# Kernel optimization log

Measured on AMD Instinct MI355X. Metric: run time of the kernel, lower is better.

The kernel has to match this reference:

```python
import jax, jax.numpy as jnp
import numpy as np
from jax import lax

N_CLASSES = 10
N_EXPERTS = 45  # 10 choose 2
EPS = 1e-5

# lookup table: (i1, i2) with i1 < i2 -> flat expert id (matches nested loop order)
_tbl = np.zeros((N_CLASSES, N_CLASSES), dtype=np.int32)
_k = 0
for _i1 in range(N_CLASSES):
    for _i2 in range(_i1 + 1, N_CLASSES):
        _tbl[_i1, _i2] = _k
        _k += 1
PAIR_TABLE = jnp.asarray(_tbl)


def _downscale(x):
    # AvgPool2d(3, stride=3) on 28x28 -> 9x9 (floor: uses top-left 27x27)
    B = x.shape[0]
    return x[:, :, :27, :27].reshape(B, 1, 9, 3, 9, 3).mean(axis=(3, 5))


def _bn_eval(h, gamma, beta, mean, var):
    scale = gamma * lax.rsqrt(var + EPS)
    return h * scale[None, :, None, None] + (beta - mean * scale)[None, :, None, None]


def _stage1(x, w1, b1, g1, be1, m1, v1, fcw1, fcb1):
    xd = _downscale(x)                                         # [B,1,9,9]
    h = lax.conv_general_dilated(xd, w1, (1, 1), 'VALID',
                                 dimension_numbers=('NCHW', 'OIHW', 'NCHW'))
    h = h + b1[None, :, None, None]                            # [B,20,7,7]
    h = _bn_eval(h, g1, be1, m1, v1)
    h = jax.nn.relu(h)
    B = h.shape[0]
    h = h[:, :, :6, :6].reshape(B, 20, 3, 2, 3, 2).max(axis=(3, 5))  # maxpool2 -> [B,20,3,3]
    h = h.reshape(B, 180)
    return h @ fcw1.T + fcb1                                   # [B,10] raw logits


def reference(x, w1, b1, g1, be1, m1, v1, fcw1, fcb1,
              w2, b2, g2, be2, m2, v2, fcw2, fcb2):
    B = x.shape[0]
    logits1 = _stage1(x, w1, b1, g1, be1, m1, v1, fcw1, fcb1)  # [B,10]
    ls1 = jax.nn.log_softmax(logits1, axis=1)

    # routing: top-2 class indices, sorted ascending, -> pairwise expert id
    top2 = jnp.sort(jnp.argsort(ls1, axis=1)[:, -2:], axis=1)  # [B,2]
    idx0, idx1 = top2[:, 0], top2[:, 1]
    eid = PAIR_TABLE[idx0, idx1]                               # [B]

    # stage 2 (TinyNet2) with per-example gathered expert params
    xd = _downscale(x)                                         # [B,1,9,9]
    # extract 5x5 conv patches (valid, stride 1): output spatial 5x5
    patches = jnp.stack([xd[:, 0, i:i + 5, j:j + 5]
                         for i in range(5) for j in range(5)], axis=1)  # [B,25,5,5]
    Wsel = w2.reshape(N_EXPERTS, 15, 25)[eid]                  # [B,15,25]
    h = jnp.einsum('bkhw,bok->bohw', patches, Wsel) + b2[eid][:, :, None, None]  # [B,15,5,5]
    scale = (g2 * lax.rsqrt(v2 + EPS))[eid]                    # [B,15]
    shift = (be2 - m2 * g2 * lax.rsqrt(v2 + EPS))[eid]
    h = h * scale[:, :, None, None] + shift[:, :, None, None]
    h = jax.nn.relu(h)
    h = h[:, :, :4, :4].reshape(B, 15, 2, 2, 2, 2).max(axis=(3, 5))  # [B,15,2,2]
    feat = h.reshape(B, 60)
    s2 = jnp.einsum('bf,bof->bo', feat, fcw2[eid]) + fcb2[eid]  # [B,2]

    # combine: scatter the two expert logits into the routed columns
    rows = jnp.arange(B)
    out = jnp.full((B, N_CLASSES), -100.0, dtype=logits1.dtype)
    out = out.at[rows, idx0].set(s2[:, 0]).at[rows, idx1].set(s2[:, 1])
    # eval-mode bypass: use stage1 raw logits if max log-prob > 0.3
    use1 = jnp.max(ls1, axis=1) > 0.3
    out = jnp.where(use1[:, None], logits1, out)
    out = jax.nn.log_softmax(out, axis=1)
    return (logits1, out)


def setup_inputs() -> dict:
    key = jax.random.key(0)
    ks = jax.random.split(key, 18)
    B = 65536
    s = 0.1
    return {
        'x': jax.random.normal(ks[0], (B, 1, 28, 28), dtype=jnp.float32),
        # stage1 (TinyNet, 20 kernels, k=3)
        'w1': jax.random.normal(ks[1], (20, 1, 3, 3), dtype=jnp.float32) * s,
        'b1': jax.random.normal(ks[2], (20,), dtype=jnp.float32) * s,
        'g1': jax.random.normal(ks[3], (20,), dtype=jnp.float32) * s + 1.0,
        'be1': jax.random.normal(ks[4], (20,), dtype=jnp.float32) * s,
        'm1': jax.random.normal(ks[5], (20,), dtype=jnp.float32) * s,
        'v1': jax.random.uniform(ks[6], (20,), dtype=jnp.float32) + 0.5,
        'fcw1': jax.random.normal(ks[7], (10, 180), dtype=jnp.float32) * s,
        'fcb1': jax.random.normal(ks[8], (10,), dtype=jnp.float32) * s,
        # 45 stacked stage2 experts (TinyNet2, 15 kernels, k=5)
        'w2': jax.random.normal(ks[9], (45, 15, 1, 5, 5), dtype=jnp.float32) * s,
        'b2': jax.random.normal(ks[10], (45, 15), dtype=jnp.float32) * s,
        'g2': jax.random.normal(ks[11], (45, 15), dtype=jnp.float32) * s + 1.0,
        'be2': jax.random.normal(ks[12], (45, 15), dtype=jnp.float32) * s,
        'm2': jax.random.normal(ks[13], (45, 15), dtype=jnp.float32) * s,
        'v2': jax.random.uniform(ks[14], (45, 15), dtype=jnp.float32) + 0.5,
        'fcw2': jax.random.normal(ks[15], (45, 2, 60), dtype=jnp.float32) * s,
        'fcb2': jax.random.normal(ks[16], (45, 2), dtype=jnp.float32) * s,
    }
```

## Files before the change

kernel.cpp:

```cpp
#include <hip/hip_runtime.h>
#include <cmath>

#define EPSF 1e-5f

#define OFF_FC2   19576
#define OFF_IMG   25088

#define I_W1P    0
#define I_FCW1R  240
#define I_B1F    2400
#define I_FCB1   2420
#define I_B2F    2432
#define I_FCB2   3108

__global__ __launch_bounds__(256) void setup_tables(
    const float* __restrict__ w1, const float* __restrict__ b1,
    const float* __restrict__ g1, const float* __restrict__ be1,
    const float* __restrict__ m1, const float* __restrict__ v1,
    const float* __restrict__ w2, const float* __restrict__ b2,
    const float* __restrict__ g2, const float* __restrict__ be2,
    const float* __restrict__ m2, const float* __restrict__ v2,
    const float* __restrict__ fcw2, const float* __restrict__ fcb2,
    const float* __restrict__ fcw1, const float* __restrict__ fcb1,
    float* __restrict__ ws)
{
  const int t  = blockIdx.x * blockDim.x + threadIdx.x;
  const int nt = gridDim.x * blockDim.x;
  float* W2F = ws;
  float* FC2 = ws + OFF_FC2;
  float* IMG = ws + OFF_IMG;

  for (int idx = t; idx < 18900; idx += nt) {
    int kk = idx & 3, rest = idx >> 2;
    int e = rest % 45, ok4 = rest / 45;
    int k4 = ok4 % 7, o = ok4 / 7;
    int k = k4 * 4 + kk;
    float s = g2[e*15+o] / sqrtf(v2[e*15+o] + EPSF);
    W2F[idx] = (k < 25) ? w2[(e*15+o)*25 + k] * s : 0.0f;
  }
  for (int idx = t; idx < 5400; idx += nt) {
    int kk = idx & 3, rest = idx >> 2;
    int e = rest % 45, t2 = rest / 45;
    int f4 = t2 % 15, oo = t2 / 15;
    FC2[idx] = fcw2[(e*2+oo)*60 + f4*4 + kk];
  }
  for (int i = t; i < 4096; i += nt) {
    float v = 0.0f;
    if (i < I_FCW1R) {
      int ch = i / 12, j = i % 12;
      if (j < 9) {
        float s = g1[ch] / sqrtf(v1[ch] + EPSF);
        v = w1[ch*9 + j] * s;
      }
    } else if (i < I_B1F) {
      int k = i - I_FCW1R;
      int c = k % 12, r2 = k / 12, pp = r2 % 9, ch = r2 / 9;
      if (c < 10) v = fcw1[c*180 + ch*9 + pp];
    } else if (i < I_FCB1) {
      int ch = i - I_B1F;
      float s = g1[ch] / sqrtf(v1[ch] + EPSF);
      v = b1[ch]*s + be1[ch] - m1[ch]*s;
    } else if (i < I_B2F) {
      int k = i - I_FCB1;
      if (k < 10) v = fcb1[k];
    } else if (i < I_FCB2) {
      int k = i - I_B2F;
      if (k < 675) {
        int e = k % 45, o = k / 45;
        float s = g2[e*15+o] / sqrtf(v2[e*15+o] + EPSF);
        v = b2[e*15+o]*s + be2[e*15+o] - m2[e*15+o]*s;
      }
    } else {
      int k = i - I_FCB2;
      if (k < 90) {
        int e = k % 45, oo = k / 45;
        v = fcb2[e*2+oo];
      }
    }
    IMG[i] = v;
  }
}

#define GETC(arr, k) ((k)%4==0 ? arr[(k)/4].x : (k)%4==1 ? arr[(k)/4].y : \
                      (k)%4==2 ? arr[(k)/4].z : arr[(k)/4].w)

#define T_RAW   4352
#define T_TAB   4352
#define SSTR    676

__global__ __attribute__((amdgpu_waves_per_eu(4, 4))) __launch_bounds__(256)
void fused_k(
    const float* __restrict__ x,
    const float* __restrict__ ws,
    float* __restrict__ out, int B)
{
  __shared__ float lds[9760];

  const int t  = threadIdx.x;
  const int p  = t & 3;
  const int sl = t >> 2;
  const int b  = blockIdx.x * 64 + sl;
  const bool valid = (b < B);

  const float4* img4 = reinterpret_cast<const float4*>(ws + OFF_IMG);
  float4 tv0 = img4[t], tv1 = img4[t + 256], tv2 = img4[t + 512], tv3 = img4[t + 768];

  const int s8  = t >> 5;
  const int tin = t & 31;

  float4 pre[6];
  {
    const int bs = blockIdx.x * 64 + s8;
    if (bs < B) {
      const float4* xp = reinterpret_cast<const float4*>(x + (size_t)bs * 784);
      #pragma unroll
      for (int j = 0; j < 5; j++) pre[j] = xp[tin + 32*j];
      pre[5] = (tin < 8) ? xp[tin + 160] : make_float4(0.f,0.f,0.f,0.f);
    } else {
      #pragma unroll
      for (int j = 0; j < 6; j++) pre[j] = make_float4(0.f,0.f,0.f,0.f);
    }
    float4* rw = reinterpret_cast<float4*>(&lds[T_RAW + s8*SSTR]);
    #pragma unroll
    for (int j = 0; j < 5; j++) rw[tin + 32*j] = pre[j];
    if (tin < 8) rw[tin + 160] = pre[5];
  }
  __syncthreads();

  #pragma unroll 1
  for (int c = 0; c < 8; c++) {
    if (c < 7) {
      const int bs = blockIdx.x * 64 + (c+1)*8 + s8;
      if (bs < B) {
        const float4* xp = reinterpret_cast<const float4*>(x + (size_t)bs * 784);
        #pragma unroll
        for (int j = 0; j < 5; j++) pre[j] = xp[tin + 32*j];
        pre[5] = (tin < 8) ? xp[tin + 160] : make_float4(0.f,0.f,0.f,0.f);
      }
    }
    if (t < 128) {
      const int ds8  = t >> 4;
      const int orow = (t >> 1) & 7;
      const int h    = t & 1;
      float a0 = 0.f, a1 = 0.f, a2 = 0.f, a3 = 0.f;
      #pragma unroll
      for (int dr = 0; dr < 3; dr++) {
        const float4* rp = reinterpret_cast<const float4*>(
            &lds[T_RAW + ds8*SSTR + (3*orow + dr)*28 + 12*h]);
        float4 q0 = rp[0], q1 = rp[1], q2 = rp[2];
        a0 += q0.x + q0.y + q0.z;
        a1 += q0.w + q1.x + q1.y;
        a2 += q1.z + q1.w + q2.x;
        a3 += q2.y + q2.z + q2.w;
      }
      float4* dst = reinterpret_cast<float4*>(&lds[(c*8 + ds8)*68 + orow*8 + 4*h]);
      *dst = make_float4(a0*(1.f/9.f), a1*(1.f/9.f), a2*(1.f/9.f), a3*(1.f/9.f));
    }
    __syncthreads();
    if (c < 7) {
      float4* rw = reinterpret_cast<float4*>(&lds[T_RAW + s8*SSTR]);
      #pragma unroll
      for (int j = 0; j < 5; j++) rw[tin + 32*j] = pre[j];
      if (tin < 8) rw[tin + 160] = pre[5];
      __syncthreads();
    }
  }

  {
    float4* tab4 = reinterpret_cast<float4*>(&lds[T_TAB]);
    tab4[t] = tv0; tab4[t + 256] = tv1; tab4[t + 512] = tv2; tab4[t + 768] = tv3;
  }

  float xd[64];
  #pragma unroll
  for (int r = 0; r < 8; r++) {
    const float4* src = reinterpret_cast<const float4*>(&lds[sl*68 + r*8]);
    float4 a = src[0], bq = src[1];
    xd[r*8+0]=a.x;  xd[r*8+1]=a.y;  xd[r*8+2]=a.z;  xd[r*8+3]=a.w;
    xd[r*8+4]=bq.x; xd[r*8+5]=bq.y; xd[r*8+6]=bq.z; xd[r*8+7]=bq.w;
  }
  __syncthreads();

  float logits[10];
  #pragma unroll
  for (int c = 0; c < 10; c++) logits[c] = 0.0f;

  #pragma unroll 1
  for (int ci = 0; ci < 5; ci++) {
    const int ch = p*5 + ci;
    const float4* wp = reinterpret_cast<const float4*>(&lds[T_TAB + I_W1P + ch*12]);
    float4 w0 = wp[0], w1v = wp[1], w2v = wp[2];
    const float w_[9] = {w0.x,w0.y,w0.z,w0.w,w1v.x,w1v.y,w1v.z,w1v.w,w2v.x};
    const float bb = lds[T_TAB + I_B1F + ch];
    float feat[9];
    #pragma unroll
    for (int pr = 0; pr < 3; pr++) {
      #pragma unroll
      for (int pc = 0; pc < 3; pc++) {
        float c00 = bb, c01 = bb, c10 = bb, c11 = bb;
        #pragma unroll
        for (int dr = 0; dr < 3; dr++) {
          #pragma unroll
          for (int dc = 0; dc < 3; dc++) {
            float wk = w_[dr*3 + dc];
            c00 = fmaf(xd[(2*pr+0+dr)*8 + 2*pc+0+dc], wk, c00);
            c01 = fmaf(xd[(2*pr+0+dr)*8 + 2*pc+1+dc], wk, c01);
            c10 = fmaf(xd[(2*pr+1+dr)*8 + 2*pc+0+dc], wk, c10);
            c11 = fmaf(xd[(2*pr+1+dr)*8 + 2*pc+1+dc], wk, c11);
          }
        }
        feat[pr*3+pc] = fmaxf(fmaxf(fmaxf(c00, c01), fmaxf(c10, c11)), 0.0f);
      }
    }
    #pragma unroll
    for (int pp = 0; pp < 9; pp++) {
      const float4* f4 = reinterpret_cast<const float4*>(&lds[T_TAB + I_FCW1R + (ch*9 + pp)*12]);
      float4 f0 = f4[0], f1 = f4[1], f2 = f4[2];
      const float fv = feat[pp];
      logits[0] = fmaf(fv, f0.x, logits[0]);
      logits[1] = fmaf(fv, f0.y, logits[1]);
      logits[2] = fmaf(fv, f0.z, logits[2]);
      logits[3] = fmaf(fv, f0.w, logits[3]);
      logits[4] = fmaf(fv, f1.x, logits[4]);
      logits[5] = fmaf(fv, f1.y, logits[5]);
      logits[6] = fmaf(fv, f1.z, logits[6]);
      logits[7] = fmaf(fv, f1.w, logits[7]);
      logits[8] = fmaf(fv, f2.x, logits[8]);
      logits[9] = fmaf(fv, f2.y, logits[9]);
    }
  }

  #pragma unroll
  for (int c = 0; c < 10; c++) {
    float v = logits[c];
    v += __shfl_xor(v, 1);
    v += __shfl_xor(v, 2);
    logits[c] = v + lds[T_TAB + I_FCB1 + c];
  }

  int i1 = 0; float v1m = logits[0];
  #pragma unroll
  for (int c = 1; c < 10; c++) { if (logits[c] >= v1m) { v1m = logits[c]; i1 = c; } }
  int i2 = 0; float v2m = -3.0e38f;
  #pragma unroll
  for (int c = 0; c < 10; c++) { if (c != i1 && logits[c] >= v2m) { v2m = logits[c]; i2 = c; } }
  const int idx0 = i1 < i2 ? i1 : i2;
  const int idx1 = i1 < i2 ? i2 : i1;
  int eid = 8*idx0 - (idx0*(idx0-1))/2 + idx1 - 1;
  eid = eid < 0 ? 0 : (eid > 44 ? 44 : eid);

  float sume = 0.0f;
  #pragma unroll
  for (int c = 0; c < 10; c++) sume += __expf(logits[c] - v1m);
  const bool use1 = (-__logf(sume)) > 0.3f;

  __syncthreads();
  if (p == 0) {
    #pragma unroll
    for (int c = 0; c < 5; c++) lds[sl*10 + c] = logits[c];
  } else if (p == 1) {
    #pragma unroll
    for (int c = 5; c < 10; c++) lds[sl*10 + c] = logits[c];
  }

  const float4* W2F4 = reinterpret_cast<const float4*>(ws);
  const float4* FC24 = reinterpret_cast<const float4*>(ws + OFF_FC2);
  float s2a = 0.0f, s2b = 0.0f;

  #pragma unroll 1
  for (int oi = 0; oi < 4; oi++) {
    const int o = p + 4*oi;
    if (o < 15) {
      float4 wv[7];
      #pragma unroll
      for (int k4 = 0; k4 < 7; k4++) wv[k4] = W2F4[(o*7 + k4)*45 + eid];
      const float bias = lds[T_TAB + I_B2F + o*45 + eid];
      const float4 fa = FC24[o*45 + eid];
      const float4 fb = FC24[(15 + o)*45 + eid];
      float feat0 = 0.f, feat1 = 0.f, feat2 = 0.f, feat3 = 0.f;
      #pragma unroll
      for (int ph = 0; ph < 2; ph++) {
        #pragma unroll
        for (int pw = 0; pw < 2; pw++) {
          float c00 = bias, c01 = bias, c10 = bias, c11 = bias;
          #pragma unroll
          for (int i = 0; i < 5; i++) {
            #pragma unroll
            for (int j = 0; j < 5; j++) {
              float wk = GETC(wv, i*5 + j);
              c00 = fmaf(xd[(2*ph+0+i)*8 + 2*pw+0+j], wk, c00);
              c01 = fmaf(xd[(2*ph+0+i)*8 + 2*pw+1+j], wk, c01);
              c10 = fmaf(xd[(2*ph+1+i)*8 + 2*pw+0+j], wk, c10);
              c11 = fmaf(xd[(2*ph+1+i)*8 + 2*pw+1+j], wk, c11);
            }
          }
          float f = fmaxf(fmaxf(fmaxf(c00, c01), fmaxf(c10, c11)), 0.0f);
          if (ph == 0 && pw == 0) feat0 = f;
          else if (ph == 0)       feat1 = f;
          else if (pw == 0)       feat2 = f;
          else                    feat3 = f;
        }
      }
      s2a = fmaf(feat0, fa.x, fmaf(feat1, fa.y, fmaf(feat2, fa.z, fmaf(feat3, fa.w, s2a))));
      s2b = fmaf(feat0, fb.x, fmaf(feat1, fb.y, fmaf(feat2, fb.z, fmaf(feat3, fb.w, s2b))));
    }
  }
  s2a += __shfl_xor(s2a, 1); s2a += __shfl_xor(s2a, 2);
  s2b += __shfl_xor(s2b, 1); s2b += __shfl_xor(s2b, 2);
  s2a += lds[T_TAB + I_FCB2 + eid];
  s2b += lds[T_TAB + I_FCB2 + 45 + eid];

  __syncthreads();
  float o10[10];
  #pragma unroll
  for (int c = 0; c < 10; c++) {
    float v = -100.0f;
    v = (c == idx0) ? s2a : v;
    v = (c == idx1) ? s2b : v;
    o10[c] = use1 ? lds[sl*10 + c] : v;
  }
  float m2x = o10[0];
  #pragma unroll
  for (int c = 1; c < 10; c++) m2x = fmaxf(m2x, o10[c]);
  float se2 = 0.0f;
  #pragma unroll
  for (int c = 0; c < 10; c++) se2 += __expf(o10[c] - m2x);
  const float lse2 = m2x + __logf(se2);

  if (p == 2) {
    #pragma unroll
    for (int c = 0; c < 5; c++) lds[640 + sl*10 + c] = o10[c] - lse2;
  } else if (p == 3) {
    #pragma unroll
    for (int c = 5; c < 10; c++) lds[640 + sl*10 + c] = o10[c] - lse2;
  }
  __syncthreads();

  if (blockIdx.x * 64 + 64 <= B) {
    const float4* l4 = reinterpret_cast<const float4*>(lds);
    const size_t o1 = (size_t)blockIdx.x * 640;
    if (t < 160)
      *reinterpret_cast<float4*>(out + o1 + (size_t)t*4) = l4[t];
    if (t >= 96)
      *reinterpret_cast<float4*>(out + (size_t)B*10 + o1 + (size_t)(t-96)*4) = l4[160 + (t-96)];
  } else if (valid) {
    const size_t base = (size_t)b * 10;
    if (p == 0) {
      #pragma unroll
      for (int c = 0; c < 5; c++) out[base + c] = lds[sl*10 + c];
    } else if (p == 1) {
      #pragma unroll
      for (int c = 5; c < 10; c++) out[base + c] = lds[sl*10 + c];
    } else if (p == 2) {
      #pragma unroll
      for (int c = 0; c < 5; c++) out[(size_t)B*10 + base + c] = lds[640 + sl*10 + c];
    } else {
      #pragma unroll
      for (int c = 5; c < 10; c++) out[(size_t)B*10 + base + c] = lds[640 + sl*10 + c];
    }
  }
}

extern "C" void kernel_launch(void* const* d_in, const int* in_sizes, int n_in,
                              void* d_out, int out_size, void* d_ws, size_t ws_size,
                              hipStream_t stream) {
  const float* x    = (const float*)d_in[0];
  const float* w1   = (const float*)d_in[1];
  const float* b1   = (const float*)d_in[2];
  const float* g1   = (const float*)d_in[3];
  const float* be1  = (const float*)d_in[4];
  const float* m1   = (const float*)d_in[5];
  const float* v1   = (const float*)d_in[6];
  const float* fcw1 = (const float*)d_in[7];
  const float* fcb1 = (const float*)d_in[8];
  const float* w2   = (const float*)d_in[9];
  const float* b2   = (const float*)d_in[10];
  const float* g2   = (const float*)d_in[11];
  const float* be2  = (const float*)d_in[12];
  const float* m2   = (const float*)d_in[13];
  const float* v2   = (const float*)d_in[14];
  const float* fcw2 = (const float*)d_in[15];
  const float* fcb2 = (const float*)d_in[16];
  float* out = (float*)d_out;
  float* ws  = (float*)d_ws;
  const int B = in_sizes[0] / 784;

  setup_tables<<<80, 256, 0, stream>>>(w1, b1, g1, be1, m1, v1,
                                       w2, b2, g2, be2, m2, v2,
                                       fcw2, fcb2, fcw1, fcb1, ws);
  fused_k<<<(B + 63)/64, 256, 0, stream>>>(x, ws, out, B);
}
```

Measured before the change: 390.1 us.

## Split work across four lanes by spatial quadrant instead of by channel

The four lanes per sample now each hold a 6x6 window of the downscaled image (36 registers instead of 64). Each lane computes one spatial quadrant for every channel in both conv stages, rather than a subset of channels over the full image. The stage-2 FC weights are repacked so each lane loads a scalar per output channel. The fixed waves-per-EU attribute is dropped, and the reduced register footprint is meant to raise occupancy. In exchange, stage 1 does redundant conv work on overlapping pooled positions, masking contributions so none are double-counted, and each lane now issues all 15 expert weight gathers instead of about four.

```diff
diff --git a/kernel.cpp b/kernel.cpp
--- a/kernel.cpp
+++ b/kernel.cpp
@@ -26,9 +26,9 @@
 {
   const int t  = blockIdx.x * blockDim.x + threadIdx.x;
   const int nt = gridDim.x * blockDim.x;
-  float* W2F = ws;
-  float* FC2 = ws + OFF_FC2;
-  float* IMG = ws + OFF_IMG;
+  float* W2F  = ws;
+  float* FC2P = ws + OFF_FC2;
+  float* IMG  = ws + OFF_IMG;
 
   for (int idx = t; idx < 18900; idx += nt) {
     int kk = idx & 3, rest = idx >> 2;
@@ -39,10 +39,10 @@
     W2F[idx] = (k < 25) ? w2[(e*15+o)*25 + k] * s : 0.0f;
   }
   for (int idx = t; idx < 5400; idx += nt) {
-    int kk = idx & 3, rest = idx >> 2;
-    int e = rest % 45, t2 = rest / 45;
-    int f4 = t2 % 15, oo = t2 / 15;
-    FC2[idx] = fcw2[(e*2+oo)*60 + f4*4 + kk];
+    int e = idx % 45, r = idx / 45;
+    int pos = r % 4, r2 = r / 4;
+    int o = r2 % 15, oo = r2 / 15;
+    FC2P[idx] = fcw2[(e*2+oo)*60 + o*4 + pos];
   }
   for (int i = t; i < 4096; i += nt) {
     float v = 0.0f;
@@ -88,8 +88,7 @@
 #define T_TAB   4352
 #define SSTR    676
 
-__global__ __attribute__((amdgpu_waves_per_eu(4, 4))) __launch_bounds__(256)
-void fused_k(
+__global__ __launch_bounds__(256) void fused_k(
     const float* __restrict__ x,
     const float* __restrict__ ws,
     float* __restrict__ out, int B)
@@ -101,9 +100,6 @@
   const int sl = t >> 2;
   const int b  = blockIdx.x * 64 + sl;
   const bool valid = (b < B);
-
-  const float4* img4 = reinterpret_cast<const float4*>(ws + OFF_IMG);
-  float4 tv0 = img4[t], tv1 = img4[t + 256], tv2 = img4[t + 512], tv3 = img4[t + 768];
 
   const int s8  = t >> 5;
   const int tin = t & 31;
@@ -166,67 +162,71 @@
     }
   }
 
+  const float4* img4 = reinterpret_cast<const float4*>(ws + OFF_IMG);
+  float4 tv0 = img4[t];
+  float4 tv1 = img4[t + 256];
+  float4 tv2 = img4[t + 512];
+  float4 tv3 = img4[t + 768];
+
+  const int R0 = p & 2;
+  const int C0 = (p & 1) * 2;
+  float xl[36];
+  #pragma unroll
+  for (int lr = 0; lr < 6; lr++) {
+    const float2* src = reinterpret_cast<const float2*>(&lds[sl*68 + (R0+lr)*8 + C0]);
+    float2 q0 = src[0], q1 = src[1], q2 = src[2];
+    xl[lr*6+0]=q0.x; xl[lr*6+1]=q0.y; xl[lr*6+2]=q1.x;
+    xl[lr*6+3]=q1.y; xl[lr*6+4]=q2.x; xl[lr*6+5]=q2.y;
+  }
   {
     float4* tab4 = reinterpret_cast<float4*>(&lds[T_TAB]);
     tab4[t] = tv0; tab4[t + 256] = tv1; tab4[t + 512] = tv2; tab4[t + 768] = tv3;
   }
-
-  float xd[64];
-  #pragma unroll
-  for (int r = 0; r < 8; r++) {
-    const float4* src = reinterpret_cast<const float4*>(&lds[sl*68 + r*8]);
-    float4 a = src[0], bq = src[1];
-    xd[r*8+0]=a.x;  xd[r*8+1]=a.y;  xd[r*8+2]=a.z;  xd[r*8+3]=a.w;
-    xd[r*8+4]=bq.x; xd[r*8+5]=bq.y; xd[r*8+6]=bq.z; xd[r*8+7]=bq.w;
-  }
-  __syncthreads();
-
+  __syncthreads();
+
+  const int basegpp = (p >> 1) * 3 + (p & 1);
   float logits[10];
   #pragma unroll
   for (int c = 0; c < 10; c++) logits[c] = 0.0f;
 
   #pragma unroll 1
-  for (int ci = 0; ci < 5; ci++) {
-    const int ch = p*5 + ci;
+  for (int ch = 0; ch < 20; ch++) {
     const float4* wp = reinterpret_cast<const float4*>(&lds[T_TAB + I_W1P + ch*12]);
     float4 w0 = wp[0], w1v = wp[1], w2v = wp[2];
     const float w_[9] = {w0.x,w0.y,w0.z,w0.w,w1v.x,w1v.y,w1v.z,w1v.w,w2v.x};
     const float bb = lds[T_TAB + I_B1F + ch];
-    float feat[9];
-    #pragma unroll
-    for (int pr = 0; pr < 3; pr++) {
-      #pragma unroll
-      for (int pc = 0; pc < 3; pc++) {
-        float c00 = bb, c01 = bb, c10 = bb, c11 = bb;
+    #pragma unroll
+    for (int lp = 0; lp < 4; lp++) {
+      const int lpr = lp >> 1, lpc = lp & 1;
+      float c00 = bb, c01 = bb, c10 = bb, c11 = bb;
+      #pragma unroll
+      for (int dr = 0; dr < 3; dr++) {
         #pragma unroll
-        for (int dr = 0; dr < 3; dr++) {
-          #pragma unroll
-          for (int dc = 0; dc < 3; dc++) {
-            float wk = w_[dr*3 + dc];
-            c00 = fmaf(xd[(2*pr+0+dr)*8 + 2*pc+0+dc], wk, c00);
-            c01 = fmaf(xd[(2*pr+0+dr)*8 + 2*pc+1+dc], wk, c01);
-            c10 = fmaf(xd[(2*pr+1+dr)*8 + 2*pc+0+dc], wk, c10);
-            c11 = fmaf(xd[(2*pr+1+dr)*8 + 2*pc+1+dc], wk, c11);
-          }
+        for (int dc = 0; dc < 3; dc++) {
+          const float wk = w_[dr*3 + dc];
+          c00 = fmaf(xl[(2*lpr+0+dr)*6 + 2*lpc+0+dc], wk, c00);
+          c01 = fmaf(xl[(2*lpr+0+dr)*6 + 2*lpc+1+dc], wk, c01);
+          c10 = fmaf(xl[(2*lpr+1+dr)*6 + 2*lpc+0+dc], wk, c10);
+          c11 = fmaf(xl[(2*lpr+1+dr)*6 + 2*lpc+1+dc], wk, c11);
         }
-        feat[pr*3+pc] = fmaxf(fmaxf(fmaxf(c00, c01), fmaxf(c10, c11)), 0.0f);
-      }
-    }
-    #pragma unroll
-    for (int pp = 0; pp < 9; pp++) {
-      const float4* f4 = reinterpret_cast<const float4*>(&lds[T_TAB + I_FCW1R + (ch*9 + pp)*12]);
+      }
+      float f = fmaxf(fmaxf(fmaxf(c00, c01), fmaxf(c10, c11)), 0.0f);
+      const int MASKS[4] = {3, 14, 5, 12};
+      const float fm = ((MASKS[lp] >> p) & 1) ? f : 0.0f;
+      const int off = (lp >> 1) * 3 + (lp & 1);
+      const float4* f4 = reinterpret_cast<const float4*>(
+          &lds[T_TAB + I_FCW1R + (ch*9 + basegpp + off)*12]);
       float4 f0 = f4[0], f1 = f4[1], f2 = f4[2];
-      const float fv = feat[pp];
-      logits[0] = fmaf(fv, f0.x, logits[0]);
-      logits[1] = fmaf(fv, f0.y, logits[1]);
-      logits[2] = fmaf(fv, f0.z, logits[2]);
-      logits[3] = fmaf(fv, f0.w, logits[3]);
-      logits[4] = fmaf(fv, f1.x, logits[4]);
-      logits[5] = fmaf(fv, f1.y, logits[5]);
-      logits[6] = fmaf(fv, f1.z, logits[6]);
-      logits[7] = fmaf(fv, f1.w, logits[7]);
-      logits[8] = fmaf(fv, f2.x, logits[8]);
-      logits[9] = fmaf(fv, f2.y, logits[9]);
+      logits[0] = fmaf(fm, f0.x, logits[0]);
+      logits[1] = fmaf(fm, f0.y, logits[1]);
+      logits[2] = fmaf(fm, f0.z, logits[2]);
+      logits[3] = fmaf(fm, f0.w, logits[3]);
+      logits[4] = fmaf(fm, f1.x, logits[4]);
+      logits[5] = fmaf(fm, f1.y, logits[5]);
+      logits[6] = fmaf(fm, f1.z, logits[6]);
+      logits[7] = fmaf(fm, f1.w, logits[7]);
+      logits[8] = fmaf(fm, f2.x, logits[8]);
+      logits[9] = fmaf(fm, f2.y, logits[9]);
     }
   }
 
@@ -264,46 +264,32 @@
   }
 
   const float4* W2F4 = reinterpret_cast<const float4*>(ws);
-  const float4* FC24 = reinterpret_cast<const float4*>(ws + OFF_FC2);
+  const float*  FC2P = ws + OFF_FC2;
   float s2a = 0.0f, s2b = 0.0f;
 
   #pragma unroll 1
-  for (int oi = 0; oi < 4; oi++) {
-    const int o = p + 4*oi;
-    if (o < 15) {
-      float4 wv[7];
-      #pragma unroll
-      for (int k4 = 0; k4 < 7; k4++) wv[k4] = W2F4[(o*7 + k4)*45 + eid];
-      const float bias = lds[T_TAB + I_B2F + o*45 + eid];
-      const float4 fa = FC24[o*45 + eid];
-      const float4 fb = FC24[(15 + o)*45 + eid];
-      float feat0 = 0.f, feat1 = 0.f, feat2 = 0.f, feat3 = 0.f;
-      #pragma unroll
-      for (int ph = 0; ph < 2; ph++) {
-        #pragma unroll
-        for (int pw = 0; pw < 2; pw++) {
-          float c00 = bias, c01 = bias, c10 = bias, c11 = bias;
-          #pragma unroll
-          for (int i = 0; i < 5; i++) {
-            #pragma unroll
-            for (int j = 0; j < 5; j++) {
-              float wk = GETC(wv, i*5 + j);
-              c00 = fmaf(xd[(2*ph+0+i)*8 + 2*pw+0+j], wk, c00);
-              c01 = fmaf(xd[(2*ph+0+i)*8 + 2*pw+1+j], wk, c01);
-              c10 = fmaf(xd[(2*ph+1+i)*8 + 2*pw+0+j], wk, c10);
-              c11 = fmaf(xd[(2*ph+1+i)*8 + 2*pw+1+j], wk, c11);
-            }
-          }
-          float f = fmaxf(fmaxf(fmaxf(c00, c01), fmaxf(c10, c11)), 0.0f);
-          if (ph == 0 && pw == 0) feat0 = f;
-          else if (ph == 0)       feat1 = f;
-          else if (pw == 0)       feat2 = f;
-          else                    feat3 = f;
-        }
-      }
-      s2a = fmaf(feat0, fa.x, fmaf(feat1, fa.y, fmaf(feat2, fa.z, fmaf(feat3, fa.w, s2a))));
-      s2b = fmaf(feat0, fb.x, fmaf(feat1, fb.y, fmaf(feat2, fb.z, fmaf(feat3, fb.w, s2b))));
-    }
+  for (int o = 0; o < 15; o++) {
+    float4 wv[7];
+    #pragma unroll
+    for (int k4 = 0; k4 < 7; k4++) wv[k4] = W2F4[(o*7 + k4)*45 + eid];
+    const float bias = lds[T_TAB + I_B2F + o*45 + eid];
+    const float fa = FC2P[(o*4 + p)*45 + eid];
+    const float fb = FC2P[((15 + o)*4 + p)*45 + eid];
+    float c00 = bias, c01 = bias, c10 = bias, c11 = bias;
+    #pragma unroll
+    for (int i = 0; i < 5; i++) {
+      #pragma unroll
+      for (int j = 0; j < 5; j++) {
+        const float wk = GETC(wv, i*5 + j);
+        c00 = fmaf(xl[(0+i)*6 + 0+j], wk, c00);
+        c01 = fmaf(xl[(0+i)*6 + 1+j], wk, c01);
+        c10 = fmaf(xl[(1+i)*6 + 0+j], wk, c10);
+        c11 = fmaf(xl[(1+i)*6 + 1+j], wk, c11);
+      }
+    }
+    const float f = fmaxf(fmaxf(fmaxf(c00, c01), fmaxf(c10, c11)), 0.0f);
+    s2a = fmaf(f, fa, s2a);
+    s2b = fmaf(f, fb, s2b);
   }
   s2a += __shfl_xor(s2a, 1); s2a += __shfl_xor(s2a, 2);
   s2b += __shfl_xor(s2b, 1); s2b += __shfl_xor(s2b, 2);
```

Measured after the change: 345.5 us. 1.13x faster.

## Halve block size to 32 samples and pack expert biases into padded weight slots

Applied to the files above, without the earlier changes.

Shrinks each block from 64 samples and 256 threads to 32 samples and 128 threads, doubling the grid and removing the fixed waves-per-EU hint in favour of launch_bounds(128,1). The stage-2 conv bias and fc2 biases now live in the padding lanes of the fused expert weight rows, so they come in with the same float4 gathers instead of separate LDS lookups. This shrinks the LDS table and frees shared memory. The table is now loaded straight into LDS at kernel start, and one barrier is removed. The risk is more blocks each paying a fixed setup cost, and a different occupancy and register balance.

```diff
diff --git a/kernel.cpp b/kernel.cpp
--- a/kernel.cpp
+++ b/kernel.cpp
@@ -3,15 +3,14 @@
 
 #define EPSF 1e-5f
 
-#define OFF_FC2   19576
-#define OFF_IMG   25088
-
-#define I_W1P    0
-#define I_FCW1R  240
-#define I_B1F    2400
-#define I_FCB1   2420
-#define I_B2F    2432
-#define I_FCB2   3108
+#define OFF_FC2 18900
+#define OFF_IMG 24300
+
+#define I_W1P   0
+#define I_FCW1R 240
+#define I_B1F   2400
+#define I_FCB1  2420
+#define IMG_SZ  2432
 
 __global__ __launch_bounds__(256) void setup_tables(
     const float* __restrict__ w1, const float* __restrict__ b1,
@@ -36,7 +35,12 @@
     int k4 = ok4 % 7, o = ok4 / 7;
     int k = k4 * 4 + kk;
     float s = g2[e*15+o] / sqrtf(v2[e*15+o] + EPSF);
-    W2F[idx] = (k < 25) ? w2[(e*15+o)*25 + k] * s : 0.0f;
+    float v;
+    if (k < 25)       v = w2[(e*15+o)*25 + k] * s;
+    else if (k == 25) v = b2[e*15+o]*s + be2[e*15+o] - m2[e*15+o]*s;
+    else if (k == 26) v = (o == 0) ? fcb2[e*2 + 0] : 0.0f;
+    else              v = (o == 0) ? fcb2[e*2 + 1] : 0.0f;
+    W2F[idx] = v;
   }
   for (int idx = t; idx < 5400; idx += nt) {
     int kk = idx & 3, rest = idx >> 2;
@@ -44,7 +48,7 @@
     int f4 = t2 % 15, oo = t2 / 15;
     FC2[idx] = fcw2[(e*2+oo)*60 + f4*4 + kk];
   }
-  for (int i = t; i < 4096; i += nt) {
+  for (int i = t; i < IMG_SZ; i += nt) {
     float v = 0.0f;
     if (i < I_FCW1R) {
       int ch = i / 12, j = i % 12;
@@ -60,22 +64,9 @@
       int ch = i - I_B1F;
       float s = g1[ch] / sqrtf(v1[ch] + EPSF);
       v = b1[ch]*s + be1[ch] - m1[ch]*s;
-    } else if (i < I_B2F) {
+    } else {
       int k = i - I_FCB1;
       if (k < 10) v = fcb1[k];
-    } else if (i < I_FCB2) {
-      int k = i - I_B2F;
-      if (k < 675) {
-        int e = k % 45, o = k / 45;
-        float s = g2[e*15+o] / sqrtf(v2[e*15+o] + EPSF);
-        v = b2[e*15+o]*s + be2[e*15+o] - m2[e*15+o]*s;
-      }
-    } else {
-      int k = i - I_FCB2;
-      if (k < 90) {
-        int e = k % 45, oo = k / 45;
-        v = fcb2[e*2+oo];
-      }
     }
     IMG[i] = v;
   }
@@ -84,33 +75,39 @@
 #define GETC(arr, k) ((k)%4==0 ? arr[(k)/4].x : (k)%4==1 ? arr[(k)/4].y : \
                       (k)%4==2 ? arr[(k)/4].z : arr[(k)/4].w)
 
-#define T_RAW   4352
-#define T_TAB   4352
-#define SSTR    676
-
-__global__ __attribute__((amdgpu_waves_per_eu(4, 4))) __launch_bounds__(256)
-void fused_k(
+#define T_RAW 2176
+#define T_TAB 4880
+#define SSTR  676
+
+__global__ __launch_bounds__(128, 1) void fused_k(
     const float* __restrict__ x,
     const float* __restrict__ ws,
     float* __restrict__ out, int B)
 {
-  __shared__ float lds[9760];
+  __shared__ float lds[7312];
 
   const int t  = threadIdx.x;
   const int p  = t & 3;
   const int sl = t >> 2;
-  const int b  = blockIdx.x * 64 + sl;
+  const int b  = blockIdx.x * 32 + sl;
   const bool valid = (b < B);
 
-  const float4* img4 = reinterpret_cast<const float4*>(ws + OFF_IMG);
-  float4 tv0 = img4[t], tv1 = img4[t + 256], tv2 = img4[t + 512], tv3 = img4[t + 768];
-
-  const int s8  = t >> 5;
+  {
+    const float4* img4 = reinterpret_cast<const float4*>(ws + OFF_IMG);
+    float4* tab4 = reinterpret_cast<float4*>(&lds[T_TAB]);
+    #pragma unroll
+    for (int k = 0; k < 5; k++) {
+      const int i = t + 128*k;
+      if (i < IMG_SZ/4) tab4[i] = img4[i];
+    }
+  }
+
+  const int s4  = t >> 5;
   const int tin = t & 31;
 
   float4 pre[6];
   {
-    const int bs = blockIdx.x * 64 + s8;
+    const int bs = blockIdx.x * 32 + s4;
     if (bs < B) {
       const float4* xp = reinterpret_cast<const float4*>(x + (size_t)bs * 784);
       #pragma unroll
@@ -120,7 +117,7 @@
       #pragma unroll
       for (int j = 0; j < 6; j++) pre[j] = make_float4(0.f,0.f,0.f,0.f);
     }
-    float4* rw = reinterpret_cast<float4*>(&lds[T_RAW + s8*SSTR]);
+    float4* rw = reinterpret_cast<float4*>(&lds[T_RAW + s4*SSTR]);
     #pragma unroll
     for (int j = 0; j < 5; j++) rw[tin + 32*j] = pre[j];
     if (tin < 8) rw[tin + 160] = pre[5];
@@ -130,7 +127,7 @@
   #pragma unroll 1
   for (int c = 0; c < 8; c++) {
     if (c < 7) {
-      const int bs = blockIdx.x * 64 + (c+1)*8 + s8;
+      const int bs = blockIdx.x * 32 + (c+1)*4 + s4;
       if (bs < B) {
         const float4* xp = reinterpret_cast<const float4*>(x + (size_t)bs * 784);
         #pragma unroll
@@ -138,37 +135,32 @@
         pre[5] = (tin < 8) ? xp[tin + 160] : make_float4(0.f,0.f,0.f,0.f);
       }
     }
-    if (t < 128) {
-      const int ds8  = t >> 4;
+    if (t < 64) {
+      const int ds4  = t >> 4;
       const int orow = (t >> 1) & 7;
       const int h    = t & 1;
       float a0 = 0.f, a1 = 0.f, a2 = 0.f, a3 = 0.f;
       #pragma unroll
       for (int dr = 0; dr < 3; dr++) {
         const float4* rp = reinterpret_cast<const float4*>(
-            &lds[T_RAW + ds8*SSTR + (3*orow + dr)*28 + 12*h]);
+            &lds[T_RAW + ds4*SSTR + (3*orow + dr)*28 + 12*h]);
         float4 q0 = rp[0], q1 = rp[1], q2 = rp[2];
         a0 += q0.x + q0.y + q0.z;
         a1 += q0.w + q1.x + q1.y;
         a2 += q1.z + q1.w + q2.x;
         a3 += q2.y + q2.z + q2.w;
       }
-      float4* dst = reinterpret_cast<float4*>(&lds[(c*8 + ds8)*68 + orow*8 + 4*h]);
+      float4* dst = reinterpret_cast<float4*>(&lds[(c*4 + ds4)*68 + orow*8 + 4*h]);
       *dst = make_float4(a0*(1.f/9.f), a1*(1.f/9.f), a2*(1.f/9.f), a3*(1.f/9.f));
     }
     __syncthreads();
     if (c < 7) {
-      float4* rw = reinterpret_cast<float4*>(&lds[T_RAW + s8*SSTR]);
+      float4* rw = reinterpret_cast<float4*>(&lds[T_RAW + s4*SSTR]);
       #pragma unroll
       for (int j = 0; j < 5; j++) rw[tin + 32*j] = pre[j];
       if (tin < 8) rw[tin + 160] = pre[5];
       __syncthreads();
     }
-  }
-
-  {
-    float4* tab4 = reinterpret_cast<float4*>(&lds[T_TAB]);
-    tab4[t] = tv0; tab4[t + 256] = tv1; tab4[t + 512] = tv2; tab4[t + 768] = tv3;
   }
 
   float xd[64];
@@ -179,7 +171,6 @@
     xd[r*8+0]=a.x;  xd[r*8+1]=a.y;  xd[r*8+2]=a.z;  xd[r*8+3]=a.w;
     xd[r*8+4]=bq.x; xd[r*8+5]=bq.y; xd[r*8+6]=bq.z; xd[r*8+7]=bq.w;
   }
-  __syncthreads();
 
   float logits[10];
   #pragma unroll
@@ -214,8 +205,9 @@
     }
     #pragma unroll
     for (int pp = 0; pp < 9; pp++) {
-      const float4* f4 = reinterpret_cast<const float4*>(&lds[T_TAB + I_FCW1R + (ch*9 + pp)*12]);
-      float4 f0 = f4[0], f1 = f4[1], f2 = f4[2];
+      const float4* f4r = reinterpret_cast<const float4*>(
+          &lds[T_TAB + I_FCW1R + (ch*9 + pp)*12]);
+      float4 f0 = f4r[0], f1 = f4r[1], f2 = f4r[2];
       const float fv = feat[pp];
       logits[0] = fmaf(fv, f0.x, logits[0]);
       logits[1] = fmaf(fv, f0.y, logits[1]);
@@ -274,9 +266,9 @@
       float4 wv[7];
       #pragma unroll
       for (int k4 = 0; k4 < 7; k4++) wv[k4] = W2F4[(o*7 + k4)*45 + eid];
-      const float bias = lds[T_TAB + I_B2F + o*45 + eid];
       const float4 fa = FC24[o*45 + eid];
       const float4 fb = FC24[(15 + o)*45 + eid];
+      const float bias = wv[6].y;
       float feat0 = 0.f, feat1 = 0.f, feat2 = 0.f, feat3 = 0.f;
       #pragma unroll
       for (int ph = 0; ph < 2; ph++) {
@@ -303,12 +295,12 @@
       }
       s2a = fmaf(feat0, fa.x, fmaf(feat1, fa.y, fmaf(feat2, fa.z, fmaf(feat3, fa.w, s2a))));
       s2b = fmaf(feat0, fb.x, fmaf(feat1, fb.y, fmaf(feat2, fb.z, fmaf(feat3, fb.w, s2b))));
+      s2a += wv[6].z;
+      s2b += wv[6].w;
     }
   }
   s2a += __shfl_xor(s2a, 1); s2a += __shfl_xor(s2a, 2);
   s2b += __shfl_xor(s2b, 1); s2b += __shfl_xor(s2b, 2);
-  s2a += lds[T_TAB + I_FCB2 + eid];
-  s2b += lds[T_TAB + I_FCB2 + 45 + eid];
 
   __syncthreads();
   float o10[10];
@@ -329,20 +321,19 @@
 
   if (p == 2) {
     #pragma unroll
-    for (int c = 0; c < 5; c++) lds[640 + sl*10 + c] = o10[c] - lse2;
+    for (int c = 0; c < 5; c++) lds[320 + sl*10 + c] = o10[c] - lse2;
   } else if (p == 3) {
     #pragma unroll
-    for (int c = 5; c < 10; c++) lds[640 + sl*10 + c] = o10[c] - lse2;
+    for (int c = 5; c < 10; c++) lds[320 + sl*10 + c] = o10[c] - lse2;
   }
   __syncthreads();
 
-  if (blockIdx.x * 64 + 64 <= B) {
+  if (blockIdx.x * 32 + 32 <= B) {
     const float4* l4 = reinterpret_cast<const float4*>(lds);
-    const size_t o1 = (size_t)blockIdx.x * 640;
-    if (t < 160)
-      *reinterpret_cast<float4*>(out + o1 + (size_t)t*4) = l4[t];
-    if (t >= 96)
-      *reinterpret_cast<float4*>(out + (size_t)B*10 + o1 + (size_t)(t-96)*4) = l4[160 + (t-96)];
+    float4* o1 = reinterpret_cast<float4*>(out + (size_t)blockIdx.x * 320);
+    float4* o2 = reinterpret_cast<float4*>(out + (size_t)B*10 + (size_t)blockIdx.x * 320);
+    if (t < 80)  o1[t] = l4[t];
+    if (t >= 48) o2[t - 48] = l4[80 + (t - 48)];
   } else if (valid) {
     const size_t base = (size_t)b * 10;
     if (p == 0) {
@@ -353,10 +344,10 @@
       for (int c = 5; c < 10; c++) out[base + c] = lds[sl*10 + c];
     } else if (p == 2) {
       #pragma unroll
-      for (int c = 0; c < 5; c++) out[(size_t)B*10 + base + c] = lds[640 + sl*10 + c];
+      for (int c = 0; c < 5; c++) out[(size_t)B*10 + base + c] = lds[320 + sl*10 + c];
     } else {
       #pragma unroll
-      for (int c = 5; c < 10; c++) out[(size_t)B*10 + base + c] = lds[640 + sl*10 + c];
+      for (int c = 5; c < 10; c++) out[(size_t)B*10 + base + c] = lds[320 + sl*10 + c];
     }
   }
 }
@@ -388,5 +379,5 @@
   setup_tables<<<80, 256, 0, stream>>>(w1, b1, g1, be1, m1, v1,
                                        w2, b2, g2, be2, m2, v2,
                                        fcw2, fcb2, fcw1, fcb1, ws);
-  fused_k<<<(B + 63)/64, 256, 0, stream>>>(x, ws, out, B);
+  fused_k<<<(B + 31)/32, 128, 0, stream>>>(x, ws, out, B);
 }
```

New measurement: 346.6 us. 1.13x faster.
